# Kernel tuning notes

Measured on AMD Instinct MI355X. Metric: run time of the kernel, lower is better.

Reference implementation:

```python
import jax, jax.numpy as jnp
import numpy as np

S = 7  # output_size
SCALES = (0.25, 0.125, 0.0625, 0.03125)


def _parallelogram_to_rectangle(rois):
    # rois: [B, N, 6] = (x, y, w, h, a, b) midpoint-offset parallelogram encoding
    x, y, w, h, a, b = [rois[..., i] for i in range(6)]
    v1 = jnp.stack([x + a, y + h / 2], -1)
    v2 = jnp.stack([x + w / 2, y + b], -1)
    v3 = jnp.stack([x - a, y - h / 2], -1)
    v4 = jnp.stack([x - w / 2, y - b], -1)
    d1 = jnp.linalg.norm(v3 - v1, axis=-1)
    d2 = jnp.linalg.norm(v4 - v2, axis=-1)
    eps = 1e-6
    cond = (d1 > d2)[..., None]
    sA = (d1 / (d2 + eps))[..., None]  # stretch v2/v4 when d1 is longer
    sB = (d2 / (d1 + eps))[..., None]  # stretch v1/v3 otherwise
    dir24 = jnp.stack([w / 2, b], -1)
    dir13 = jnp.stack([a, h / 2], -1)
    v2n = v2 + (sA - 1.0) * dir24
    v4n = v4 - (sA - 1.0) * dir24
    v1n = v1 + (sB - 1.0) * dir13
    v3n = v3 - (sB - 1.0) * dir13
    V0 = jnp.where(cond, v1, v1n)
    V1 = jnp.where(cond, v2n, v2)
    V2 = jnp.where(cond, v3, v3n)
    h_rect = jnp.linalg.norm(V1 - V0, axis=-1)
    w_rect = jnp.linalg.norm(V2 - V1, axis=-1)
    theta = jnp.arctan2(V1[..., 1] - V2[..., 1], V1[..., 0] - V2[..., 0])
    theta = jnp.clip(theta, -np.pi / 2, np.pi / 2)
    return x, y, w_rect, h_rect, theta  # each [B, N]


def _bilinear_sample(feat, px, py):
    # feat: [B, C, H, W]; px, py: [B, N, S, S] pixel coords; border padding
    B, C, H, W = feat.shape
    x0f = jnp.floor(px)
    y0f = jnp.floor(py)
    wx = (px - x0f)[:, None]  # [B, 1, N, S, S] broadcast over channels
    wy = (py - y0f)[:, None]
    x0 = jnp.clip(x0f.astype(jnp.int32), 0, W - 1)
    x1 = jnp.clip(x0 + 1, 0, W - 1)
    y0 = jnp.clip(y0f.astype(jnp.int32), 0, H - 1)
    y1 = jnp.clip(y0 + 1, 0, H - 1)
    flat = feat.reshape(B, C, H * W)
    nss = px.shape[1:]  # (N, S, S)

    def gat(yi, xi):
        idx = (yi * W + xi).reshape(B, -1)  # [B, N*S*S]
        v = jax.vmap(lambda f, i: jnp.take(f, i, axis=1))(flat, idx)  # [B, C, N*S*S]
        return v.reshape(B, C, *nss)

    v00 = gat(y0, x0)
    v01 = gat(y0, x1)
    v10 = gat(y1, x0)
    v11 = gat(y1, x1)
    out = (v00 * (1 - wx) * (1 - wy) + v01 * wx * (1 - wy)
           + v10 * (1 - wx) * wy + v11 * wx * wy)  # [B, C, N, S, S]
    return out.transpose(0, 2, 1, 3, 4)  # [B, N, C, S, S]


def rotated_roi_align(feats, rois, levels):
    x, y, w_rect, h_rect, theta = _parallelogram_to_rectangle(rois)  # [B, N]
    B, N = x.shape
    t = jnp.arange(S, dtype=rois.dtype) / (S - 1) - 0.5  # linspace(-1/2, 1/2, S)
    c = jnp.cos(theta)[:, :, None, None]
    s_ = jnp.sin(theta)[:, :, None, None]
    out = jnp.zeros((B, N, feats[0].shape[1], S, S), rois.dtype)
    for l, (feat, scale) in enumerate(zip(feats, SCALES)):
        H, W = feat.shape[2], feat.shape[3]
        x_r = (x * scale)[:, :, None, None]
        y_r = (y * scale)[:, :, None, None]
        w_r = (w_rect * scale)[:, :, None, None]
        h_r = (h_rect * scale)[:, :, None, None]
        gx = w_r * t[None, None, None, :]  # columns vary x
        gy = h_r * t[None, None, :, None]  # rows vary y
        rx = gx * c + gy * s_ + x_r  # grid @ [[c,-s],[s,c]]
        ry = -gx * s_ + gy * c + y_r
        # faithful to source: grid scaled by spatial_scale a second time,
        # align_corners=True-style normalization then align_corners=False unmap
        gxn = rx * scale / max(W - 1, 1) * 2 - 1
        gyn = ry * scale / max(H - 1, 1) * 2 - 1
        px = ((gxn + 1) * W - 1) / 2
        py = ((gyn + 1) * H - 1) / 2
        cand = _bilinear_sample(feat, px, py)  # [B, N, C, S, S]
        out = jnp.where(levels[:, :, None, None, None] == l, cand, out)
    return out


def setup_inputs() -> dict:
    key = jax.random.key(0)
    ks = jax.random.split(key, 6)
    B, C, N = 2, 256, 512
    f0 = jax.random.normal(ks[0], (B, C, 256, 256), jnp.float32)
    f1 = jax.random.normal(ks[1], (B, C, 128, 128), jnp.float32)
    f2 = jax.random.normal(ks[2], (B, C, 64, 64), jnp.float32)
    f3 = jax.random.normal(ks[3], (B, C, 32, 32), jnp.float32)
    u = jax.random.uniform(ks[4], (B, N, 6), jnp.float32)
    cx = 100 + 800 * u[..., 0]
    cy = 100 + 800 * u[..., 1]
    w = 32 + 224 * u[..., 2]
    h = 32 + 224 * u[..., 3]
    a = (u[..., 4] - 0.5) * 0.5 * w  # |dalpha| <= w/4
    b = (u[..., 5] - 0.5) * 0.5 * h  # |dbeta|  <= h/4
    rois = jnp.stack([cx, cy, w, h, a, b], -1)
    levels = jax.random.randint(ks[5], (B, N), 0, 4, dtype=jnp.int32)
    return {"f0": f0, "f1": f1, "f2": f2, "f3": f3, "rois": rois, "levels": levels}


def reference(f0, f1, f2, f3, rois, levels):
    return rotated_roi_align([f0, f1, f2, f3], rois, levels)  # [B, N, C, 7, 7]
```

## Files before the change

kernel.cpp:

```cpp
#include <hip/hip_runtime.h>
#include <math.h>

#define S 7
#define NPOS 49
#define CCH 256

__global__ __launch_bounds__(256) void rroi_align_kernel(
    const float* __restrict__ f0, const float* __restrict__ f1,
    const float* __restrict__ f2, const float* __restrict__ f3,
    const float* __restrict__ rois, const int* __restrict__ levels,
    float* __restrict__ out, int N)
{
    const int bn  = blockIdx.x;
    const int b   = bn / N;
    const int tid = threadIdx.x;

    const float* r = rois + (size_t)bn * 6;
    const float x = r[0], y = r[1], w = r[2], h = r[3], a = r[4], bb = r[5];

    const float v1x = x + a,       v1y = y + 0.5f * h;
    const float v2x = x + 0.5f * w, v2y = y + bb;
    const float v3x = x - a,       v3y = y - 0.5f * h;
    const float v4x = x - 0.5f * w, v4y = y - bb;
    const float d1 = sqrtf((v3x - v1x) * (v3x - v1x) + (v3y - v1y) * (v3y - v1y));
    const float d2 = sqrtf((v4x - v2x) * (v4x - v2x) + (v4y - v2y) * (v4y - v2y));
    const float eps = 1e-6f;
    const bool  cond = d1 > d2;
    const float sA = d1 / (d2 + eps);
    const float sB = d2 / (d1 + eps);
    const float d24x = 0.5f * w, d24y = bb;
    const float d13x = a,        d13y = 0.5f * h;
    const float v2nx = v2x + (sA - 1.f) * d24x, v2ny = v2y + (sA - 1.f) * d24y;
    const float v1nx = v1x + (sB - 1.f) * d13x, v1ny = v1y + (sB - 1.f) * d13y;
    const float v3nx = v3x - (sB - 1.f) * d13x, v3ny = v3y - (sB - 1.f) * d13y;
    const float V0x = cond ? v1x : v1nx, V0y = cond ? v1y : v1ny;
    const float V1x = cond ? v2nx : v2x, V1y = cond ? v2ny : v2y;
    const float V2x = cond ? v3x : v3nx, V2y = cond ? v3y : v3ny;
    const float h_rect = sqrtf((V1x - V0x) * (V1x - V0x) + (V1y - V0y) * (V1y - V0y));
    const float w_rect = sqrtf((V2x - V1x) * (V2x - V1x) + (V2y - V1y) * (V2y - V1y));
    float theta = atan2f(V1y - V2y, V1x - V2x);
    const float HPI = 1.5707963267948966f;
    theta = fminf(fmaxf(theta, -HPI), HPI);

    const int lvl = levels[bn];
    const float* feat; int H, W; float scale;
    switch (lvl) {
      case 0:  feat = f0; H = 256; W = 256; scale = 0.25f;    break;
      case 1:  feat = f1; H = 128; W = 128; scale = 0.125f;   break;
      case 2:  feat = f2; H = 64;  W = 64;  scale = 0.0625f;  break;
      default: feat = f3; H = 32;  W = 32;  scale = 0.03125f; break;
    }

    __shared__ int   sx0[NPOS], sx1[NPOS], sy0[NPOS], sy1[NPOS];
    __shared__ float swx[NPOS], swy[NPOS];

    if (tid < NPOS) {
        const int iy = tid / S, ix = tid - iy * S;
        const float tI = (float)ix / (float)(S - 1) - 0.5f;
        const float tJ = (float)iy / (float)(S - 1) - 0.5f;
        const float c_ = cosf(theta), s_ = sinf(theta);
        const float x_r = x * scale, y_r = y * scale;
        const float gx = (w_rect * scale) * tI;
        const float gy = (h_rect * scale) * tJ;
        const float rx =  gx * c_ + gy * s_ + x_r;
        const float ry = -gx * s_ + gy * c_ + y_r;
        const float gxn = rx * scale / (float)(W - 1) * 2.f - 1.f;
        const float gyn = ry * scale / (float)(H - 1) * 2.f - 1.f;
        const float px = ((gxn + 1.f) * (float)W - 1.f) * 0.5f;
        const float py = ((gyn + 1.f) * (float)H - 1.f) * 0.5f;
        const float x0f = floorf(px), y0f = floorf(py);
        swx[tid] = px - x0f;
        swy[tid] = py - y0f;
        int x0 = (int)x0f; x0 = min(max(x0, 0), W - 1);
        int y0 = (int)y0f; y0 = min(max(y0, 0), H - 1);
        sx0[tid] = x0;
        sx1[tid] = min(x0 + 1, W - 1);
        sy0[tid] = y0;
        sy1[tid] = min(y0 + 1, H - 1);
    }
    __syncthreads();

    const size_t plane = (size_t)H * W;
    const float* fb = feat + (size_t)b * CCH * plane;
    float* ob = out + (size_t)bn * CCH * NPOS;

    #pragma unroll 1
    for (int k = 0; k < NPOS; ++k) {
        const int idx = k * 256 + tid;
        const int c   = idx / NPOS;
        const int pos = idx - c * NPOS;
        const int   x0 = sx0[pos], x1 = sx1[pos];
        const int   y0 = sy0[pos], y1 = sy1[pos];
        const float wx = swx[pos], wy = swy[pos];
        const float* fc = fb + (size_t)c * plane;
        const float v00 = fc[y0 * W + x0];
        const float v01 = fc[y0 * W + x1];
        const float v10 = fc[y1 * W + x0];
        const float v11 = fc[y1 * W + x1];
        ob[idx] = v00 * (1.f - wx) * (1.f - wy)
                + v01 * wx         * (1.f - wy)
                + v10 * (1.f - wx) * wy
                + v11 * wx         * wy;
    }
}

extern "C" void kernel_launch(void* const* d_in, const int* in_sizes, int n_in,
                              void* d_out, int out_size, void* d_ws, size_t ws_size,
                              hipStream_t stream) {
    const float* f0   = (const float*)d_in[0];
    const float* f1   = (const float*)d_in[1];
    const float* f2   = (const float*)d_in[2];
    const float* f3   = (const float*)d_in[3];
    const float* rois = (const float*)d_in[4];
    const int*   lev  = (const int*)d_in[5];
    float* out = (float*)d_out;

    const int total_bn = in_sizes[5];
    const int B = in_sizes[0] / (CCH * 256 * 256);
    const int N = total_bn / B;

    rroi_align_kernel<<<total_bn, 256, 0, stream>>>(f0, f1, f2, f3, rois, lev, out, N);
}
```

Measured before the change: 245.7 us.

## Split channels across grid y, precompute bilinear offsets/weights, unroll gather loop

Launches a 2D grid that gives each ROI four blocks, with each block handling a quarter of the channels. This multiplies block count to raise occupancy and latency hiding. Shared memory now holds precomputed flat offsets and the four combined bilinear weights, which cuts per-element index math. The gather loop is unrolled by 4 for more memory-level parallelism, and a tail block covers the remainder. The ROI geometry is now recomputed once per channel split, which adds a little redundant work.

```diff
diff --git a/kernel.cpp b/kernel.cpp
--- a/kernel.cpp
+++ b/kernel.cpp
@@ -4,6 +4,11 @@
 #define S 7
 #define NPOS 49
 #define CCH 256
+#define CSPLIT 4
+#define CPB (CCH / CSPLIT)
+#define OUTPB (CPB * NPOS)
+#define KFULL (OUTPB / 256)
+#define KTAIL (OUTPB - KFULL * 256)
 
 __global__ __launch_bounds__(256) void rroi_align_kernel(
     const float* __restrict__ f0, const float* __restrict__ f1,
@@ -12,15 +17,16 @@
     float* __restrict__ out, int N)
 {
     const int bn  = blockIdx.x;
+    const int q   = blockIdx.y;
     const int b   = bn / N;
     const int tid = threadIdx.x;
 
     const float* r = rois + (size_t)bn * 6;
     const float x = r[0], y = r[1], w = r[2], h = r[3], a = r[4], bb = r[5];
 
-    const float v1x = x + a,       v1y = y + 0.5f * h;
+    const float v1x = x + a,        v1y = y + 0.5f * h;
     const float v2x = x + 0.5f * w, v2y = y + bb;
-    const float v3x = x - a,       v3y = y - 0.5f * h;
+    const float v3x = x - a,        v3y = y - 0.5f * h;
     const float v4x = x - 0.5f * w, v4y = y - bb;
     const float d1 = sqrtf((v3x - v1x) * (v3x - v1x) + (v3y - v1y) * (v3y - v1y));
     const float d2 = sqrtf((v4x - v2x) * (v4x - v2x) + (v4y - v2y) * (v4y - v2y));
@@ -51,8 +57,8 @@
       default: feat = f3; H = 32;  W = 32;  scale = 0.03125f; break;
     }
 
-    __shared__ int   sx0[NPOS], sx1[NPOS], sy0[NPOS], sy1[NPOS];
-    __shared__ float swx[NPOS], swy[NPOS];
+    __shared__ int   so00[NPOS], so01[NPOS], so10[NPOS], so11[NPOS];
+    __shared__ float sw00[NPOS], sw01[NPOS], sw10[NPOS], sw11[NPOS];
 
     if (tid < NPOS) {
         const int iy = tid / S, ix = tid - iy * S;
@@ -69,38 +75,54 @@
         const float px = ((gxn + 1.f) * (float)W - 1.f) * 0.5f;
         const float py = ((gyn + 1.f) * (float)H - 1.f) * 0.5f;
         const float x0f = floorf(px), y0f = floorf(py);
-        swx[tid] = px - x0f;
-        swy[tid] = py - y0f;
+        const float wx = px - x0f, wy = py - y0f;
         int x0 = (int)x0f; x0 = min(max(x0, 0), W - 1);
         int y0 = (int)y0f; y0 = min(max(y0, 0), H - 1);
-        sx0[tid] = x0;
-        sx1[tid] = min(x0 + 1, W - 1);
-        sy0[tid] = y0;
-        sy1[tid] = min(y0 + 1, H - 1);
+        const int x1 = min(x0 + 1, W - 1);
+        const int y1 = min(y0 + 1, H - 1);
+        so00[tid] = y0 * W + x0;
+        so01[tid] = y0 * W + x1;
+        so10[tid] = y1 * W + x0;
+        so11[tid] = y1 * W + x1;
+        sw00[tid] = (1.f - wx) * (1.f - wy);
+        sw01[tid] = wx         * (1.f - wy);
+        sw10[tid] = (1.f - wx) * wy;
+        sw11[tid] = wx         * wy;
     }
     __syncthreads();
 
     const size_t plane = (size_t)H * W;
-    const float* fb = feat + (size_t)b * CCH * plane;
-    float* ob = out + (size_t)bn * CCH * NPOS;
+    const float* fb = feat + ((size_t)b * CCH + (size_t)q * CPB) * plane;
+    float* ob = out + (size_t)bn * CCH * NPOS + (size_t)q * OUTPB;
 
-    #pragma unroll 1
-    for (int k = 0; k < NPOS; ++k) {
+    #pragma unroll 4
+    for (int k = 0; k < KFULL; ++k) {
         const int idx = k * 256 + tid;
         const int c   = idx / NPOS;
         const int pos = idx - c * NPOS;
-        const int   x0 = sx0[pos], x1 = sx1[pos];
-        const int   y0 = sy0[pos], y1 = sy1[pos];
-        const float wx = swx[pos], wy = swy[pos];
         const float* fc = fb + (size_t)c * plane;
-        const float v00 = fc[y0 * W + x0];
-        const float v01 = fc[y0 * W + x1];
-        const float v10 = fc[y1 * W + x0];
-        const float v11 = fc[y1 * W + x1];
-        ob[idx] = v00 * (1.f - wx) * (1.f - wy)
-                + v01 * wx         * (1.f - wy)
-                + v10 * (1.f - wx) * wy
-                + v11 * wx         * wy;
+        const float v00 = fc[so00[pos]];
+        const float v01 = fc[so01[pos]];
+        const float v10 = fc[so10[pos]];
+        const float v11 = fc[so11[pos]];
+        ob[idx] = fmaf(v00, sw00[pos],
+                  fmaf(v01, sw01[pos],
+                  fmaf(v10, sw10[pos],
+                       v11 * sw11[pos])));
+    }
+    if (tid < KTAIL) {
+        const int idx = KFULL * 256 + tid;
+        const int c   = idx / NPOS;
+        const int pos = idx - c * NPOS;
+        const float* fc = fb + (size_t)c * plane;
+        const float v00 = fc[so00[pos]];
+        const float v01 = fc[so01[pos]];
+        const float v10 = fc[so10[pos]];
+        const float v11 = fc[so11[pos]];
+        ob[idx] = fmaf(v00, sw00[pos],
+                  fmaf(v01, sw01[pos],
+                  fmaf(v10, sw10[pos],
+                       v11 * sw11[pos])));
     }
 }
 
@@ -119,5 +141,6 @@
     const int B = in_sizes[0] / (CCH * 256 * 256);
     const int N = total_bn / B;
 
-    rroi_align_kernel<<<total_bn, 256, 0, stream>>>(f0, f1, f2, f3, rois, lev, out, N);
+    dim3 grid(total_bn, CSPLIT);
+    rroi_align_kernel<<<grid, 256, 0, stream>>>(f0, f1, f2, f3, rois, lev, out, N);
 }
```

Measured after the change: 235.5 us. 4.2% less time.
